# Optimization experiments

Hardware: AMD Instinct MI355X
Metric: run time of the kernel (lower is better)

## Reference

```python
import jax, jax.numpy as jnp
import numpy as np

B, T, E, H, D = 256, 77, 1280, 20, 64
SCALE = D ** -0.5
NEG = -1e9


def setup_inputs() -> dict:
    key = jax.random.key(0)
    ks = jax.random.split(key, 32)
    w = lambda k, shape, s=0.02: jax.random.normal(k, shape, dtype=jnp.float32) * s
    causal = jnp.triu(jnp.full((T, T), NEG, dtype=jnp.float32), k=1)
    causal_mask = jnp.broadcast_to(causal[None, None], (B, 1, T, T))
    return {
        'hidden_states': jax.random.normal(ks[0], (B, T, E), dtype=jnp.float32),
        'embeds': jax.random.normal(ks[1], (B, T, E), dtype=jnp.float32),
        'causal_mask': causal_mask,
        'q_w': w(ks[2], (E, E)), 'q_b': w(ks[3], (E,)),
        'k_w': w(ks[4], (E, E)), 'k_b': w(ks[5], (E,)),
        'v_w': w(ks[6], (E, E)), 'v_b': w(ks[7], (E,)),
        'o_w': w(ks[8], (E, E)), 'o_b': w(ks[9], (E,)),
        'ka_w': w(ks[10], (E, E)) * 0.01, 'ka_b': w(ks[11], (E,)) * 0.001,
        'va_w': w(ks[12], (E, E)) * 0.01, 'va_b': w(ks[13], (E,)) * 0.001,
        'zc1_w': w(ks[14], (E, E)), 'zc1_b': w(ks[15], (E,)),
        'zt1_w': w(ks[16], (T, 2 * T)), 'zt1_b': w(ks[17], (T,)),
        'zc2_w': w(ks[18], (E, E)), 'zc2_b': w(ks[19], (E,)),
        'zt2_w': w(ks[20], (T, T)), 'zt2_b': w(ks[21], (T,)),
    }


def _heads(x):
    # (B, S, E) -> (B, H, S, D)
    return x.reshape(B, -1, H, D).transpose(0, 2, 1, 3)


def _attend(q, k, v, mask=None):
    # q,k,v: (B,H,*,D); returns (B,T,E)
    logits = jnp.einsum('bhtd,bhsd->bhts', q, k)
    if mask is not None:
        logits = logits + mask  # mask: (B,1,T,S)
    probs = jax.nn.softmax(logits, axis=-1)  # dropout p=0 in eval
    ctx = jnp.einsum('bhts,bhsd->bhtd', probs, v)
    return ctx.transpose(0, 2, 1, 3).reshape(B, T, E)


def _zipper(x, zc1_w, zc1_b, zt1_w, zt1_b, zc2_w, zc2_b, zt2_w, zt2_b):
    # token/channel mixer: (B, 2T, E) -> (B, T, E)
    x = jax.nn.gelu(x @ zc1_w.T + zc1_b)              # channel: E -> hidden E
    x = jnp.swapaxes(x, 1, 2)                          # (B, E, 2T)
    x = jax.nn.gelu(x @ zt1_w.T + zt1_b)               # tokens: 2T -> T
    x = jnp.swapaxes(x, 1, 2)                          # (B, T, E)
    x = x @ zc2_w.T + zc2_b                            # channel: E -> E
    x = jnp.swapaxes(x, 1, 2) @ zt2_w.T + zt2_b        # tokens: T -> T
    return jnp.swapaxes(x, 1, 2)


def reference(hidden_states, embeds, causal_mask,
              q_w, q_b, k_w, k_b, v_w, v_b, o_w, o_b,
              ka_w, ka_b, va_w, va_b,
              zc1_w, zc1_b, zt1_w, zt1_b, zc2_w, zc2_b, zt2_w, zt2_b):
    q = _heads((hidden_states @ q_w.T + q_b) * SCALE)
    k = _heads(hidden_states @ k_w.T + k_b)
    v = _heads(hidden_states @ v_w.T + v_b)
    attn_output = _attend(q, k, v, causal_mask)  # self-attention pass

    # adapter cross-attention pass (shared query)
    ka = _heads(embeds @ ka_w.T + ka_b)
    va = _heads(embeds @ va_w.T + va_b)
    attn_output_adapter = _attend(q, ka, va, None)

    zipped = _zipper(jnp.concatenate([attn_output_adapter, attn_output], axis=1),
                     zc1_w, zc1_b, zt1_w, zt1_b, zc2_w, zc2_b, zt2_w, zt2_b)
    attn_output = attn_output + zipped
    return attn_output @ o_w.T + o_b
```

## Files before the change

kernel.cpp:

```cpp
#include <hip/hip_runtime.h>
#include <stdint.h>

#define B_    256
#define T_    77
#define E_    1280
#define H_    20
#define T2_   154
#define MTOK  19712
#define MTOK2 39424

typedef float f32x4 __attribute__((ext_vector_type(4)));
typedef short bf16x8 __attribute__((ext_vector_type(8)));

__device__ inline float bf2f(short s) {
    return __uint_as_float(((unsigned)(unsigned short)s) << 16);
}
__device__ inline short f2bf(float f) {
    unsigned u = __float_as_uint(f);
    u += 0x7fff + ((u >> 16) & 1);
    return (short)(u >> 16);
}
__device__ inline float gelu_tanh(float x) {
    float x3 = x * x * x;
    return 0.5f * x * (1.0f + tanhf(0.7978845608028654f * (x + 0.044715f * x3)));
}

__global__ void cast_f32_bf16(const float* __restrict__ in, short* __restrict__ out, int n4) {
    int i = blockIdx.x * blockDim.x + threadIdx.x;
    int stride = gridDim.x * blockDim.x;
    for (; i < n4; i += stride) {
        float4 v = reinterpret_cast<const float4*>(in)[i];
        short4 o;
        o.x = f2bf(v.x); o.y = f2bf(v.y); o.z = f2bf(v.z); o.w = f2bf(v.w);
        reinterpret_cast<short4*>(out)[i] = o;
    }
}

__global__ void pad_weight(const float* __restrict__ W, short* __restrict__ Wp,
                           int rows, int cols, int KP) {
    int i = blockIdx.x * 256 + threadIdx.x;
    if (i >= 80 * KP) return;
    int t = i / KP, s = i - t * KP;
    Wp[i] = (t < rows && s < cols) ? f2bf(W[t * cols + s]) : (short)0;
}

template<int EPI>
__global__ void gemm_bt(const short* __restrict__ A, const short* __restrict__ W,
                        const float* __restrict__ bias, void* __restrict__ Cout,
                        int K, float scale) {
    const int N = E_;
    const int NBN = E_ / 128;
    __shared__ short Als[128 * 64];
    __shared__ short Bls[128 * 64];
    const int tid  = threadIdx.x;
    const int wave = tid >> 6, lane = tid & 63;

    const int nwg = gridDim.x;
    const int qq = nwg >> 3, rr = nwg & 7;
    const int x = blockIdx.x & 7, ii = blockIdx.x >> 3;
    const int L = (x < rr ? x * (qq + 1) : rr * (qq + 1) + (x - rr) * qq) + ii;
    const int bm = L / NBN, bn = L % NBN;

    const int wm = (wave >> 1) * 64, wn = (wave & 1) * 64;

    f32x4 acc[4][4] = {};

    const long arow0 = (long)bm * 128;
    const long brow0 = (long)bn * 128;
    const int rsub = lane >> 3;
    const int col  = (((lane & 7) ^ rsub) & 7) * 8;
    const int swz  = (lane & 7) << 3;

    for (int kt = 0; kt < K; kt += 64) {
        __syncthreads();
#pragma unroll
        for (int i = 0; i < 4; ++i) {
            int chunk = i * 4 + wave;
            int row = chunk * 8 + rsub;
            const short* ga = A + (arow0 + row) * K + kt + col;
            const short* gb = W + (brow0 + row) * K + kt + col;
            __builtin_amdgcn_global_load_lds(
                (const __attribute__((address_space(1))) unsigned int*)ga,
                (__attribute__((address_space(3))) unsigned int*)&Als[chunk * 512], 16, 0, 0);
            __builtin_amdgcn_global_load_lds(
                (const __attribute__((address_space(1))) unsigned int*)gb,
                (__attribute__((address_space(3))) unsigned int*)&Bls[chunk * 512], 16, 0, 0);
        }
        __syncthreads();
#pragma unroll
        for (int kk = 0; kk < 2; ++kk) {
            bf16x8 af[4], bfr[4];
#pragma unroll
            for (int mi = 0; mi < 4; ++mi)
                af[mi] = *reinterpret_cast<const bf16x8*>(
                    &Als[(((wm + mi * 16 + (lane & 15)) * 64 + kk * 32 + (lane >> 4) * 8)) ^ swz]);
#pragma unroll
            for (int nj = 0; nj < 4; ++nj)
                bfr[nj] = *reinterpret_cast<const bf16x8*>(
                    &Bls[(((wn + nj * 16 + (lane & 15)) * 64 + kk * 32 + (lane >> 4) * 8)) ^ swz]);
#pragma unroll
            for (int mi = 0; mi < 4; ++mi)
#pragma unroll
                for (int nj = 0; nj < 4; ++nj)
                    acc[mi][nj] = __builtin_amdgcn_mfma_f32_16x16x32_bf16(
                        af[mi], bfr[nj], acc[mi][nj], 0, 0, 0);
        }
    }

#pragma unroll
    for (int mi = 0; mi < 4; ++mi) {
#pragma unroll
        for (int nj = 0; nj < 4; ++nj) {
            int gcol = bn * 128 + wn + nj * 16 + (lane & 15);
            float bv = bias[gcol];
#pragma unroll
            for (int r = 0; r < 4; ++r) {
                long grow = arow0 + wm + mi * 16 + (lane >> 4) * 4 + r;
                float v = acc[mi][nj][r] + bv;
                if (EPI == 1) v *= scale;
                if (EPI == 2) v = gelu_tanh(v);
                if (EPI == 3) ((float*)Cout)[grow * N + gcol] = v;
                else          ((short*)Cout)[grow * N + gcol] = f2bf(v);
            }
        }
    }
}

template<int SIN, int KP, int PS, bool GELU, bool RESID>
__global__ void mixer_mfma(const short* __restrict__ IN, const short* __restrict__ Wp,
                           const float* __restrict__ bias, const short* __restrict__ Cat,
                           short* __restrict__ OUT) {
    __shared__ short lsT[64 * PS];
    const int e0 = blockIdx.x * 64;
    const int b  = blockIdx.y;
    const int tid = threadIdx.x, wave = tid >> 6, lane = tid & 63;

    const int eg = tid & 7;
    const int sl = tid >> 3;
    for (int sb = sl; sb < KP; sb += 32) {
        if (sb < SIN) {
            bf16x8 v = *reinterpret_cast<const bf16x8*>(
                &IN[((long)b * SIN + sb) * E_ + e0 + eg * 8]);
#pragma unroll
            for (int i = 0; i < 8; ++i)
                lsT[(eg * 8 + i) * PS + sb] = v[i];
        } else {
#pragma unroll
            for (int i = 0; i < 8; ++i)
                lsT[(eg * 8 + i) * PS + sb] = 0;
        }
    }
    __syncthreads();

    const int ebase = wave * 16;
    f32x4 acc[5] = {};
#pragma unroll
    for (int ks = 0; ks < KP / 32; ++ks) {
        bf16x8 bfr = *reinterpret_cast<const bf16x8*>(
            &lsT[(ebase + (lane & 15)) * PS + ks * 32 + (lane >> 4) * 8]);
#pragma unroll
        for (int mt = 0; mt < 5; ++mt) {
            bf16x8 af = *reinterpret_cast<const bf16x8*>(
                &Wp[(mt * 16 + (lane & 15)) * KP + ks * 32 + (lane >> 4) * 8]);
            acc[mt] = __builtin_amdgcn_mfma_f32_16x16x32_bf16(af, bfr, acc[mt], 0, 0, 0);
        }
    }

    const int e = e0 + ebase + (lane & 15);
#pragma unroll
    for (int mt = 0; mt < 5; ++mt) {
#pragma unroll
        for (int r = 0; r < 4; ++r) {
            int t = mt * 16 + (lane >> 4) * 4 + r;
            if (t < T_) {
                float v = acc[mt][r] + bias[t];
                if (GELU) v = gelu_tanh(v);
                if (RESID) v += bf2f(Cat[((long)b * T2_ + T_ + t) * E_ + e]);
                OUT[((long)b * T_ + t) * E_ + e] = f2bf(v);
            }
        }
    }
}

#define ASTR 104
__global__ __launch_bounds__(64, 1)
void attn_mfma(const short* __restrict__ Qm,
               const short* __restrict__ Km, const short* __restrict__ Vm,
               const short* __restrict__ KAm, const short* __restrict__ VAm,
               short* __restrict__ Cat) {
    __shared__ short pls[80 * ASTR];
    __shared__ short vt[64 * ASTR];
    const int hh = blockIdx.x;
    const int b = hh / H_, h = hh % H_;
    const int lane = threadIdx.x & 63;
    const int colbase = lane & 15, g = lane >> 4;
    const long base = ((long)b * T_) * E_ + h * 64;

    for (int pass = 0; pass < 2; ++pass) {
        const short* Kp = pass ? KAm : Km;
        const short* Vp = pass ? VAm : Vm;
        const bool causal = (pass == 0);
        const int rowoff = pass ? 0 : T_;

        {
            int4 z = {0, 0, 0, 0};
#pragma unroll
            for (int it = 0; it < 4; ++it) {
                int idx = it * 64 + lane;
                int row = idx >> 2, cb = idx & 3;
                *reinterpret_cast<int4*>(&vt[row * ASTR + 64 + cb * 8]) = z;
            }
#pragma unroll
            for (int it = 0; it < 3; ++it) {
                int idx = it * 64 + lane;
                if (idx < 160) {
                    int row = idx >> 1, cb = idx & 1;
                    *reinterpret_cast<int4*>(&pls[row * ASTR + 80 + cb * 8]) = z;
                }
            }
        }

        {
            const short* vb = Vp + base + (long)lane * E_;
#pragma unroll
            for (int dg = 0; dg < 8; ++dg) {
                bf16x8 v = *reinterpret_cast<const bf16x8*>(vb + dg * 8);
#pragma unroll
                for (int i = 0; i < 8; ++i) vt[(dg * 8 + i) * ASTR + lane] = v[i];
            }
            if (lane < T_ - 64) {
                const short* vb2 = Vp + base + (long)(64 + lane) * E_;
#pragma unroll
                for (int dg = 0; dg < 8; ++dg) {
                    bf16x8 v = *reinterpret_cast<const bf16x8*>(vb2 + dg * 8);
#pragma unroll
                    for (int i = 0; i < 8; ++i) vt[(dg * 8 + i) * ASTR + 64 + lane] = v[i];
                }
            }
        }

        f32x4 sacc[5][5] = {};
#pragma unroll
        for (int kk = 0; kk < 2; ++kk) {
            bf16x8 qf[5];
#pragma unroll
            for (int mi = 0; mi < 5; ++mi) {
                int t = mi * 16 + colbase; t = t > 76 ? 76 : t;
                qf[mi] = *reinterpret_cast<const bf16x8*>(
                    Qm + base + (long)t * E_ + kk * 32 + g * 8);
            }
#pragma unroll
            for (int nj = 0; nj < 5; ++nj) {
                int s = nj * 16 + colbase; s = s > 76 ? 76 : s;
                bf16x8 kf = *reinterpret_cast<const bf16x8*>(
                    Kp + base + (long)s * E_ + kk * 32 + g * 8);
#pragma unroll
                for (int mi = 0; mi < 5; ++mi)
                    sacc[mi][nj] = __builtin_amdgcn_mfma_f32_16x16x32_bf16(
                        qf[mi], kf, sacc[mi][nj], 0, 0, 0);
            }
        }

        float inv[5][4];
#pragma unroll
        for (int mi = 0; mi < 5; ++mi) {
#pragma unroll
            for (int r = 0; r < 4; ++r) {
                int t = mi * 16 + g * 4 + r;
                float mx = -3.0e38f;
#pragma unroll
                for (int nj = 0; nj < 5; ++nj) {
                    int s = nj * 16 + colbase;
                    bool ok = causal ? (s <= t) : (s < T_);
                    if (ok) mx = fmaxf(mx, sacc[mi][nj][r]);
                }
#pragma unroll
                for (int o = 1; o <= 8; o <<= 1) mx = fmaxf(mx, __shfl_xor(mx, o));
                float sum = 0.f;
#pragma unroll
                for (int nj = 0; nj < 5; ++nj) {
                    int s = nj * 16 + colbase;
                    bool ok = causal ? (s <= t) : (s < T_);
                    float pv = ok ? __expf(sacc[mi][nj][r] - mx) : 0.f;
                    sacc[mi][nj][r] = pv;
                    sum += pv;
                }
#pragma unroll
                for (int o = 1; o <= 8; o <<= 1) sum += __shfl_xor(sum, o);
                inv[mi][r] = 1.0f / sum;
            }
        }

#pragma unroll
        for (int mi = 0; mi < 5; ++mi)
#pragma unroll
            for (int nj = 0; nj < 5; ++nj)
#pragma unroll
                for (int r = 0; r < 4; ++r)
                    pls[(mi * 16 + g * 4 + r) * ASTR + nj * 16 + colbase] =
                        f2bf(sacc[mi][nj][r]);

        f32x4 cacc[5][4] = {};
#pragma unroll
        for (int ks = 0; ks < 3; ++ks) {
            bf16x8 pa[5];
#pragma unroll
            for (int mi = 0; mi < 5; ++mi)
                pa[mi] = *reinterpret_cast<const bf16x8*>(
                    &pls[(mi * 16 + colbase) * ASTR + ks * 32 + g * 8]);
#pragma unroll
            for (int nd = 0; nd < 4; ++nd) {
                bf16x8 vf = *reinterpret_cast<const bf16x8*>(
                    &vt[(nd * 16 + colbase) * ASTR + ks * 32 + g * 8]);
#pragma unroll
                for (int mi = 0; mi < 5; ++mi)
                    cacc[mi][nd] = __builtin_amdgcn_mfma_f32_16x16x32_bf16(
                        pa[mi], vf, cacc[mi][nd], 0, 0, 0);
            }
        }

#pragma unroll
        for (int mi = 0; mi < 5; ++mi)
#pragma unroll
            for (int nd = 0; nd < 4; ++nd)
#pragma unroll
                for (int r = 0; r < 4; ++r) {
                    int t = mi * 16 + g * 4 + r;
                    if (t < T_) {
                        float val = cacc[mi][nd][r] * inv[mi][r];
                        Cat[((long)b * T2_ + rowoff + t) * E_ + h * 64 + nd * 16 + colbase] =
                            f2bf(val);
                    }
                }
    }
}

extern "C" void kernel_launch(void* const* d_in, const int* in_sizes, int n_in,
                              void* d_out, int out_size, void* d_ws, size_t ws_size,
                              hipStream_t stream) {
    const float* hidden = (const float*)d_in[0];
    const float* embeds = (const float*)d_in[1];
    const float* q_w  = (const float*)d_in[3];  const float* q_b  = (const float*)d_in[4];
    const float* k_w  = (const float*)d_in[5];  const float* k_b  = (const float*)d_in[6];
    const float* v_w  = (const float*)d_in[7];  const float* v_b  = (const float*)d_in[8];
    const float* o_w  = (const float*)d_in[9];  const float* o_b  = (const float*)d_in[10];
    const float* ka_w = (const float*)d_in[11]; const float* ka_b = (const float*)d_in[12];
    const float* va_w = (const float*)d_in[13]; const float* va_b = (const float*)d_in[14];
    const float* zc1_w = (const float*)d_in[15]; const float* zc1_b = (const float*)d_in[16];
    const float* zt1_w = (const float*)d_in[17]; const float* zt1_b = (const float*)d_in[18];
    const float* zc2_w = (const float*)d_in[19]; const float* zc2_b = (const float*)d_in[20];
    const float* zt2_w = (const float*)d_in[21]; const float* zt2_b = (const float*)d_in[22];

    char* ws = (char*)d_ws;
    const size_t WSZ = (size_t)E_ * E_ * 2;
    const size_t ASZ = (size_t)MTOK * E_ * 2;
    short* Wq  = (short*)(ws + 0 * WSZ);
    short* Wk  = (short*)(ws + 1 * WSZ);
    short* Wv  = (short*)(ws + 2 * WSZ);
    short* Wka = (short*)(ws + 3 * WSZ);
    short* Wva = (short*)(ws + 4 * WSZ);
    short* Wz1 = (short*)(ws + 5 * WSZ);
    short* Wz2 = (short*)(ws + 6 * WSZ);
    short* Wo  = (short*)(ws + 7 * WSZ);
    char* p = ws + 8 * WSZ;
    short* Ahs  = (short*)p; p += ASZ;
    short* Aemb = (short*)p; p += ASZ;
    short* Qb   = (short*)p; p += ASZ;
    short* Kb   = (short*)p; p += ASZ;
    short* Vb   = (short*)p; p += ASZ;
    short* KAb  = (short*)p; p += ASZ;
    short* VAb  = (short*)p; p += ASZ;
    short* Wz1p = (short*)p; p += 80 * 160 * 2;
    short* Wz2p = (short*)p; p += 80 * 96 * 2;
    short* CAT = Ahs;
    short* Y   = KAb;
    short* X2  = Qb;
    short* X3  = Kb;
    short* S   = Vb;

    if (ws_size < (size_t)(p - ws)) return;

    cast_f32_bf16<<<2048, 256, 0, stream>>>(hidden, Ahs,  MTOK * E_ / 4);
    cast_f32_bf16<<<2048, 256, 0, stream>>>(embeds, Aemb, MTOK * E_ / 4);
    cast_f32_bf16<<<512, 256, 0, stream>>>(q_w,  Wq,  E_ * E_ / 4);
    cast_f32_bf16<<<512, 256, 0, stream>>>(k_w,  Wk,  E_ * E_ / 4);
    cast_f32_bf16<<<512, 256, 0, stream>>>(v_w,  Wv,  E_ * E_ / 4);
    cast_f32_bf16<<<512, 256, 0, stream>>>(ka_w, Wka, E_ * E_ / 4);
    cast_f32_bf16<<<512, 256, 0, stream>>>(va_w, Wva, E_ * E_ / 4);
    cast_f32_bf16<<<512, 256, 0, stream>>>(zc1_w, Wz1, E_ * E_ / 4);
    cast_f32_bf16<<<512, 256, 0, stream>>>(zc2_w, Wz2, E_ * E_ / 4);
    cast_f32_bf16<<<512, 256, 0, stream>>>(o_w,  Wo,  E_ * E_ / 4);
    pad_weight<<<(80 * 160 + 255) / 256, 256, 0, stream>>>(zt1_w, Wz1p, 77, 154, 160);
    pad_weight<<<(80 * 96 + 255) / 256, 256, 0, stream>>>(zt2_w, Wz2p, 77, 77, 96);

    const int g154 = (MTOK / 128) * (E_ / 128);
    const int g308 = (MTOK2 / 128) * (E_ / 128);
    gemm_bt<1><<<g154, 256, 0, stream>>>(Ahs,  Wq,  q_b,  Qb,  E_, 0.125f);
    gemm_bt<0><<<g154, 256, 0, stream>>>(Ahs,  Wk,  k_b,  Kb,  E_, 1.f);
    gemm_bt<0><<<g154, 256, 0, stream>>>(Ahs,  Wv,  v_b,  Vb,  E_, 1.f);
    gemm_bt<0><<<g154, 256, 0, stream>>>(Aemb, Wka, ka_b, KAb, E_, 1.f);
    gemm_bt<0><<<g154, 256, 0, stream>>>(Aemb, Wva, va_b, VAb, E_, 1.f);
    attn_mfma<<<B_ * H_, 64, 0, stream>>>(Qb, Kb, Vb, KAb, VAb, CAT);
    gemm_bt<2><<<g308, 256, 0, stream>>>(CAT, Wz1, zc1_b, Y, E_, 1.f);
    mixer_mfma<154, 160, 168, true, false><<<dim3(E_ / 64, B_), 256, 0, stream>>>(
        Y, Wz1p, zt1_b, nullptr, X2);
    gemm_bt<0><<<g154, 256, 0, stream>>>(X2, Wz2, zc2_b, X3, E_, 1.f);
    mixer_mfma<77, 96, 104, false, true><<<dim3(E_ / 64, B_), 256, 0, stream>>>(
        X3, Wz2p, zt2_b, CAT, S);
    gemm_bt<3><<<g154, 256, 0, stream>>>(S, Wo, o_b, (float*)d_out, E_, 1.f);
}
```

Baseline: 1.048 ms.

## Double-buffer GEMM LDS tiles with 256x128 blocks and 512 threads

Rewrites the bf16 projection GEMM to use 256x128 output tiles computed by 8 waves, with double-buffered LDS so the global-to-LDS loads for the next K step are issued while the current step's MFMAs run. It also uses manual vmcnt waits and raises wave priority around the MFMA block. The aim is to hide global load latency and raise arithmetic intensity per tile. The cost is 96KB of LDS per block, which allows at most one or two blocks per CU, plus more accumulator registers per wave and fewer blocks overall (77x10 and 154x10).

```diff
diff --git a/kernel.cpp b/kernel.cpp
--- a/kernel.cpp
+++ b/kernel.cpp
@@ -8,6 +8,10 @@
 #define T2_   154
 #define MTOK  19712
 #define MTOK2 39424
+
+#define BM2 256
+#define BN2 128
+#define BK2 64
 
 typedef float f32x4 __attribute__((ext_vector_type(4)));
 typedef short bf16x8 __attribute__((ext_vector_type(8)));
@@ -45,13 +49,14 @@
 }
 
 template<int EPI>
-__global__ void gemm_bt(const short* __restrict__ A, const short* __restrict__ W,
-                        const float* __restrict__ bias, void* __restrict__ Cout,
-                        int K, float scale) {
+__global__ __launch_bounds__(512, 2)
+void gemm_bt(const short* __restrict__ A, const short* __restrict__ W,
+             const float* __restrict__ bias, void* __restrict__ Cout,
+             int K, float scale) {
     const int N = E_;
-    const int NBN = E_ / 128;
-    __shared__ short Als[128 * 64];
-    __shared__ short Bls[128 * 64];
+    const int NBN = E_ / BN2;
+    __shared__ short Als[2][BM2 * BK2];
+    __shared__ short Bls[2][BN2 * BK2];
     const int tid  = threadIdx.x;
     const int wave = tid >> 6, lane = tid & 63;
 
@@ -61,61 +66,85 @@
     const int L = (x < rr ? x * (qq + 1) : rr * (qq + 1) + (x - rr) * qq) + ii;
     const int bm = L / NBN, bn = L % NBN;
 
-    const int wm = (wave >> 1) * 64, wn = (wave & 1) * 64;
-
-    f32x4 acc[4][4] = {};
-
-    const long arow0 = (long)bm * 128;
-    const long brow0 = (long)bn * 128;
-    const int rsub = lane >> 3;
-    const int col  = (((lane & 7) ^ rsub) & 7) * 8;
+    const int wr = wave >> 2, wc = wave & 3;
+
+    f32x4 acc[8][2] = {};
+
+    const long arow0 = (long)bm * BM2;
+    const long brow0 = (long)bn * BN2;
+    const int trow = tid >> 3;
+    const int tcol = (((tid & 7) ^ ((tid >> 3) & 7))) * 8;
     const int swz  = (lane & 7) << 3;
-
-    for (int kt = 0; kt < K; kt += 64) {
-        __syncthreads();
-#pragma unroll
-        for (int i = 0; i < 4; ++i) {
-            int chunk = i * 4 + wave;
-            int row = chunk * 8 + rsub;
-            const short* ga = A + (arow0 + row) * K + kt + col;
-            const short* gb = W + (brow0 + row) * K + kt + col;
+    const int NT = K / BK2;
+
+    auto ISSUE = [&](int kt) {
+        const int b = kt & 1;
+        const short* ab = A + arow0 * K + kt * BK2;
+#pragma unroll
+        for (int r = 0; r < 4; ++r) {
+            const short* ga = ab + (long)(r * 64 + trow) * K + tcol;
             __builtin_amdgcn_global_load_lds(
                 (const __attribute__((address_space(1))) unsigned int*)ga,
-                (__attribute__((address_space(3))) unsigned int*)&Als[chunk * 512], 16, 0, 0);
+                (__attribute__((address_space(3))) unsigned int*)&Als[b][r * 4096 + wave * 512],
+                16, 0, 0);
+        }
+        const short* bb = W + brow0 * K + kt * BK2;
+#pragma unroll
+        for (int r = 0; r < 2; ++r) {
+            const short* gb = bb + (long)(r * 64 + trow) * K + tcol;
             __builtin_amdgcn_global_load_lds(
                 (const __attribute__((address_space(1))) unsigned int*)gb,
-                (__attribute__((address_space(3))) unsigned int*)&Bls[chunk * 512], 16, 0, 0);
-        }
-        __syncthreads();
+                (__attribute__((address_space(3))) unsigned int*)&Bls[b][r * 4096 + wave * 512],
+                16, 0, 0);
+        }
+    };
+
+    ISSUE(0);
+    for (int kt = 0; kt < NT; ++kt) {
+        if (kt + 1 < NT) {
+            ISSUE(kt + 1);
+            asm volatile("s_waitcnt vmcnt(6)" ::: "memory");
+        } else {
+            asm volatile("s_waitcnt vmcnt(0)" ::: "memory");
+        }
+        __builtin_amdgcn_sched_barrier(0);
+        __builtin_amdgcn_s_barrier();
+
+        const short* Ab = Als[kt & 1];
+        const short* Bb = Bls[kt & 1];
 #pragma unroll
         for (int kk = 0; kk < 2; ++kk) {
-            bf16x8 af[4], bfr[4];
-#pragma unroll
-            for (int mi = 0; mi < 4; ++mi)
+            bf16x8 af[8], bfr[2];
+#pragma unroll
+            for (int mi = 0; mi < 8; ++mi)
                 af[mi] = *reinterpret_cast<const bf16x8*>(
-                    &Als[(((wm + mi * 16 + (lane & 15)) * 64 + kk * 32 + (lane >> 4) * 8)) ^ swz]);
-#pragma unroll
-            for (int nj = 0; nj < 4; ++nj)
+                    &Ab[((wr * 128 + mi * 16 + (lane & 15)) * 64 + kk * 32 + (lane >> 4) * 8) ^ swz]);
+#pragma unroll
+            for (int nj = 0; nj < 2; ++nj)
                 bfr[nj] = *reinterpret_cast<const bf16x8*>(
-                    &Bls[(((wn + nj * 16 + (lane & 15)) * 64 + kk * 32 + (lane >> 4) * 8)) ^ swz]);
-#pragma unroll
-            for (int mi = 0; mi < 4; ++mi)
-#pragma unroll
-                for (int nj = 0; nj < 4; ++nj)
+                    &Bb[((wc * 32 + nj * 16 + (lane & 15)) * 64 + kk * 32 + (lane >> 4) * 8) ^ swz]);
+            __builtin_amdgcn_s_setprio(1);
+#pragma unroll
+            for (int mi = 0; mi < 8; ++mi)
+#pragma unroll
+                for (int nj = 0; nj < 2; ++nj)
                     acc[mi][nj] = __builtin_amdgcn_mfma_f32_16x16x32_bf16(
                         af[mi], bfr[nj], acc[mi][nj], 0, 0, 0);
-        }
-    }
-
-#pragma unroll
-    for (int mi = 0; mi < 4; ++mi) {
-#pragma unroll
-        for (int nj = 0; nj < 4; ++nj) {
-            int gcol = bn * 128 + wn + nj * 16 + (lane & 15);
+            __builtin_amdgcn_s_setprio(0);
+        }
+        __builtin_amdgcn_sched_barrier(0);
+        __builtin_amdgcn_s_barrier();
+    }
+
+#pragma unroll
+    for (int mi = 0; mi < 8; ++mi) {
+#pragma unroll
+        for (int nj = 0; nj < 2; ++nj) {
+            int gcol = bn * BN2 + wc * 32 + nj * 16 + (lane & 15);
             float bv = bias[gcol];
 #pragma unroll
             for (int r = 0; r < 4; ++r) {
-                long grow = arow0 + wm + mi * 16 + (lane >> 4) * 4 + r;
+                long grow = arow0 + wr * 128 + mi * 16 + (lane >> 4) * 4 + r;
                 float v = acc[mi][nj][r] + bv;
                 if (EPI == 1) v *= scale;
                 if (EPI == 2) v = gelu_tanh(v);
@@ -393,19 +422,19 @@
     pad_weight<<<(80 * 160 + 255) / 256, 256, 0, stream>>>(zt1_w, Wz1p, 77, 154, 160);
     pad_weight<<<(80 * 96 + 255) / 256, 256, 0, stream>>>(zt2_w, Wz2p, 77, 77, 96);
 
-    const int g154 = (MTOK / 128) * (E_ / 128);
-    const int g308 = (MTOK2 / 128) * (E_ / 128);
-    gemm_bt<1><<<g154, 256, 0, stream>>>(Ahs,  Wq,  q_b,  Qb,  E_, 0.125f);
-    gemm_bt<0><<<g154, 256, 0, stream>>>(Ahs,  Wk,  k_b,  Kb,  E_, 1.f);
-    gemm_bt<0><<<g154, 256, 0, stream>>>(Ahs,  Wv,  v_b,  Vb,  E_, 1.f);
-    gemm_bt<0><<<g154, 256, 0, stream>>>(Aemb, Wka, ka_b, KAb, E_, 1.f);
-    gemm_bt<0><<<g154, 256, 0, stream>>>(Aemb, Wva, va_b, VAb, E_, 1.f);
+    const int g154 = (MTOK / BM2) * (E_ / BN2);
+    const int g308 = (MTOK2 / BM2) * (E_ / BN2);
+    gemm_bt<1><<<g154, 512, 0, stream>>>(Ahs,  Wq,  q_b,  Qb,  E_, 0.125f);
+    gemm_bt<0><<<g154, 512, 0, stream>>>(Ahs,  Wk,  k_b,  Kb,  E_, 1.f);
+    gemm_bt<0><<<g154, 512, 0, stream>>>(Ahs,  Wv,  v_b,  Vb,  E_, 1.f);
+    gemm_bt<0><<<g154, 512, 0, stream>>>(Aemb, Wka, ka_b, KAb, E_, 1.f);
+    gemm_bt<0><<<g154, 512, 0, stream>>>(Aemb, Wva, va_b, VAb, E_, 1.f);
     attn_mfma<<<B_ * H_, 64, 0, stream>>>(Qb, Kb, Vb, KAb, VAb, CAT);
-    gemm_bt<2><<<g308, 256, 0, stream>>>(CAT, Wz1, zc1_b, Y, E_, 1.f);
+    gemm_bt<2><<<g308, 512, 0, stream>>>(CAT, Wz1, zc1_b, Y, E_, 1.f);
     mixer_mfma<154, 160, 168, true, false><<<dim3(E_ / 64, B_), 256, 0, stream>>>(
         Y, Wz1p, zt1_b, nullptr, X2);
-    gemm_bt<0><<<g154, 256, 0, stream>>>(X2, Wz2, zc2_b, X3, E_, 1.f);
+    gemm_bt<0><<<g154, 512, 0, stream>>>(X2, Wz2, zc2_b, X3, E_, 1.f);
     mixer_mfma<77, 96, 104, false, true><<<dim3(E_ / 64, B_), 256, 0, stream>>>(
         X3, Wz2p, zt2_b, CAT, S);
-    gemm_bt<3><<<g154, 256, 0, stream>>>(S, Wo, o_b, (float*)d_out, E_, 1.f);
-}
+    gemm_bt<3><<<g154, 512, 0, stream>>>(S, Wo, o_b, (float*)d_out, E_, 1.f);
+}
```

After: 1.491 ms. 42.3% more time.
